# Performance work log

Measured on AMD Instinct MI355X. Metric: run time of the kernel, lower is better.

## Reference

```python
import jax, jax.numpy as jnp
import numpy as np

N0 = 260000  # all sampled nodes (hop-2 sources)
N1 = 60000   # hop-1 targets / hop-2 sources
N2 = 10000   # final batch targets
E1 = 1500000
E2 = 250000
DIN, DH, DOUT = 128, 256, 128


def sage_conv(x_src, x_tgt, src, dst, n_tgt, Wl, b, Wr):
    # mean aggregation of source features over incoming edges per target,
    # then lin_l(agg) + lin_r(x_tgt)  (PyG SAGEConv default, lin_r has no bias)
    msg = x_src[src]                                             # [E, d]
    agg = jax.ops.segment_sum(msg, dst, num_segments=n_tgt)      # [n_tgt, d]
    cnt = jax.ops.segment_sum(jnp.ones((src.shape[0], 1), x_src.dtype), dst,
                              num_segments=n_tgt)                # [n_tgt, 1]
    agg = agg / jnp.maximum(cnt, 1.0)
    return agg @ Wl + b + x_tgt @ Wr


def setup_inputs() -> dict:
    key = jax.random.key(0)
    ks = jax.random.split(key, 10)
    s = 1.0 / np.sqrt(DIN)
    s2 = 1.0 / np.sqrt(DH)
    return {
        "x": jax.random.normal(ks[0], (N0, DIN), dtype=jnp.float32),
        "W1l": jax.random.normal(ks[1], (DIN, DH), dtype=jnp.float32) * s,
        "b1": jnp.zeros((DH,), dtype=jnp.float32),
        "W1r": jax.random.normal(ks[2], (DIN, DH), dtype=jnp.float32) * s,
        "W2l": jax.random.normal(ks[3], (DH, DOUT), dtype=jnp.float32) * s2,
        "b2": jnp.zeros((DOUT,), dtype=jnp.float32),
        "W2r": jax.random.normal(ks[4], (DH, DOUT), dtype=jnp.float32) * s2,
        "src1": jax.random.randint(ks[5], (E1,), 0, N0, dtype=jnp.int32),
        "dst1": jax.random.randint(ks[6], (E1,), 0, N1, dtype=jnp.int32),
        "src2": jax.random.randint(ks[7], (E2,), 0, N1, dtype=jnp.int32),
        "dst2": jax.random.randint(ks[8], (E2,), 0, N2, dtype=jnp.int32),
    }


def reference(x, W1l, b1, W1r, W2l, b2, W2r, src1, dst1, src2, dst2):
    h = sage_conv(x, x[:N1], src1, dst1, N1, W1l, b1, W1r)  # [N1, DH]
    h = jax.nn.relu(h)
    out = sage_conv(h, h[:N2], src2, dst2, N2, W2l, b2, W2r)  # [N2, DOUT]
    return out
```

## Files before the change

### kernel.cpp

```cpp
#include <hip/hip_runtime.h>
#include <hip/hip_bf16.h>

#define N0 260000
#define N1 60000
#define N2 10000
#define E1 1500000
#define E2 250000
#define DIN 128
#define DH 256
#define DOUT 128
#define CAP 80

typedef __attribute__((ext_vector_type(8))) short bf16x8;
typedef __attribute__((ext_vector_type(4))) float f32x4;

#define MFMA16(a, b, c) __builtin_amdgcn_mfma_f32_16x16x32_bf16(a, b, c, 0, 0, 0)

__device__ inline float blo(unsigned u) { return __uint_as_float(u << 16); }
__device__ inline float bhi(unsigned u) { return __uint_as_float(u & 0xFFFF0000u); }
__device__ inline unsigned short f2b(float f) {
    unsigned u = __float_as_uint(f);
    return (unsigned short)((u + 0x7FFFu + ((u >> 16) & 1u)) >> 16);
}

#define BB_C1 256
#define BB_C2 64
#define BB_BLOCKS (8 * (BB_C1 + BB_C2))
#define P1ROWS (N1 / 8)
#define P2ROWS (N2 / 8)
#define CONVX_BLOCKS 16250
#define CONVW_BLOCKS 512
__global__ __launch_bounds__(256) void prep3(const float* __restrict__ x, unsigned short* __restrict__ xb,
                                             const float* __restrict__ W1l, const float* __restrict__ W1r,
                                             const float* __restrict__ W2l, const float* __restrict__ W2r,
                                             unsigned short* __restrict__ W1lt, unsigned short* __restrict__ W1rt,
                                             unsigned short* __restrict__ W2lt, unsigned short* __restrict__ W2rt,
                                             const int* __restrict__ src1, const int* __restrict__ dst1,
                                             int* __restrict__ cnt1, int* __restrict__ csr1,
                                             const int* __restrict__ src2, const int* __restrict__ dst2,
                                             int* __restrict__ cnt2, int* __restrict__ csr2,
                                             int use_xb) {
    int b = blockIdx.x;
    int t = threadIdx.x;
    if (b < BB_BLOCKS) {
        int part = b & 7, q = b >> 3;
        if (q < BB_C1) {
            int lo = part * P1ROWS, hi = lo + P1ROWS;
            const int4* d4 = reinterpret_cast<const int4*>(dst1);
            for (int i = q * 256 + t; i < E1 / 4; i += BB_C1 * 256) {
                int4 d = d4[i];
                int e0 = i * 4;
                if (d.x >= lo && d.x < hi) { int p = atomicAdd(&cnt1[d.x], 1); if (p < CAP) csr1[d.x * CAP + p] = src1[e0 + 0]; }
                if (d.y >= lo && d.y < hi) { int p = atomicAdd(&cnt1[d.y], 1); if (p < CAP) csr1[d.y * CAP + p] = src1[e0 + 1]; }
                if (d.z >= lo && d.z < hi) { int p = atomicAdd(&cnt1[d.z], 1); if (p < CAP) csr1[d.z * CAP + p] = src1[e0 + 2]; }
                if (d.w >= lo && d.w < hi) { int p = atomicAdd(&cnt1[d.w], 1); if (p < CAP) csr1[d.w * CAP + p] = src1[e0 + 3]; }
            }
        } else {
            q -= BB_C1;
            int lo = part * P2ROWS, hi = lo + P2ROWS;
            const int4* d4 = reinterpret_cast<const int4*>(dst2);
            for (int i = q * 256 + t; i < E2 / 4; i += BB_C2 * 256) {
                int4 d = d4[i];
                int e0 = i * 4;
                if (d.x >= lo && d.x < hi) { int p = atomicAdd(&cnt2[d.x], 1); if (p < CAP) csr2[d.x * CAP + p] = src2[e0 + 0]; }
                if (d.y >= lo && d.y < hi) { int p = atomicAdd(&cnt2[d.y], 1); if (p < CAP) csr2[d.y * CAP + p] = src2[e0 + 1]; }
                if (d.z >= lo && d.z < hi) { int p = atomicAdd(&cnt2[d.z], 1); if (p < CAP) csr2[d.z * CAP + p] = src2[e0 + 2]; }
                if (d.w >= lo && d.w < hi) { int p = atomicAdd(&cnt2[d.w], 1); if (p < CAP) csr2[d.w * CAP + p] = src2[e0 + 3]; }
            }
        }
    } else if (b < BB_BLOCKS + CONVX_BLOCKS) {
        if (!use_xb) return;
        size_t i = (size_t)(b - BB_BLOCKS) * 256 + t;
        const float4* xf = reinterpret_cast<const float4*>(x) + i * 2;
        float4 v0 = xf[0], v1 = xf[1];
        bf16x8 o;
        o[0] = (short)f2b(v0.x); o[1] = (short)f2b(v0.y); o[2] = (short)f2b(v0.z); o[3] = (short)f2b(v0.w);
        o[4] = (short)f2b(v1.x); o[5] = (short)f2b(v1.y); o[6] = (short)f2b(v1.z); o[7] = (short)f2b(v1.w);
        *reinterpret_cast<bf16x8*>(xb + i * 8) = o;
    } else {
        int tid = (b - BB_BLOCKS - CONVX_BLOCKS) * 256 + t;
        int seg = tid >> 15, idx = tid & 32767;
        if (seg == 0)      { int n = idx >> 7, k = idx & 127; W1lt[idx] = f2b(W1l[k * DH + n]); }
        else if (seg == 1) { int n = idx >> 7, k = idx & 127; W1rt[idx] = f2b(W1r[k * DH + n]); }
        else if (seg == 2) { int n = idx >> 8, k = idx & 255; W2lt[idx] = f2b(W2l[k * DOUT + n]); }
        else               { int n = idx >> 8, k = idx & 255; W2rt[idx] = f2b(W2r[k * DOUT + n]); }
    }
}

template <int XB>
__global__ __launch_bounds__(256) void agg_gemm1_k(const float* __restrict__ xf,
                                                   const unsigned short* __restrict__ xb,
                                                   const int* __restrict__ cnt,
                                                   const int* __restrict__ csr,
                                                   const unsigned short* __restrict__ Wlt,
                                                   const unsigned short* __restrict__ Wrt,
                                                   const float* __restrict__ b1,
                                                   unsigned short* __restrict__ hb) {
    __shared__ __align__(16) unsigned short lds[4352];
    const int XT0 = 2176;
    int t = threadIdx.x;
    int row0 = blockIdx.x * 16;
    int r = t >> 4, li = t & 15;
    int rawc = cnt[row0 + r];
    int deg = rawc > CAP ? CAP : rawc;
    int beg = (row0 + r) * CAP, end = beg + deg;
    float acc[8];
#pragma unroll
    for (int j = 0; j < 8; ++j) acc[j] = 0.0f;
    if (XB) {
        const uint4* base = reinterpret_cast<const uint4*>(xb);
        int e = beg;
        for (; e + 8 <= end; e += 8) {
            int4 sa = *reinterpret_cast<const int4*>(csr + e);
            int4 sb = *reinterpret_cast<const int4*>(csr + e + 4);
            uint4 v0 = base[(size_t)sa.x * 16 + li];
            uint4 v1 = base[(size_t)sa.y * 16 + li];
            uint4 v2 = base[(size_t)sa.z * 16 + li];
            uint4 v3 = base[(size_t)sa.w * 16 + li];
            uint4 v4 = base[(size_t)sb.x * 16 + li];
            uint4 v5 = base[(size_t)sb.y * 16 + li];
            uint4 v6 = base[(size_t)sb.z * 16 + li];
            uint4 v7 = base[(size_t)sb.w * 16 + li];
            acc[0] += blo(v0.x) + blo(v1.x) + blo(v2.x) + blo(v3.x) + blo(v4.x) + blo(v5.x) + blo(v6.x) + blo(v7.x);
            acc[1] += bhi(v0.x) + bhi(v1.x) + bhi(v2.x) + bhi(v3.x) + bhi(v4.x) + bhi(v5.x) + bhi(v6.x) + bhi(v7.x);
            acc[2] += blo(v0.y) + blo(v1.y) + blo(v2.y) + blo(v3.y) + blo(v4.y) + blo(v5.y) + blo(v6.y) + blo(v7.y);
            acc[3] += bhi(v0.y) + bhi(v1.y) + bhi(v2.y) + bhi(v3.y) + bhi(v4.y) + bhi(v5.y) + bhi(v6.y) + bhi(v7.y);
            acc[4] += blo(v0.z) + blo(v1.z) + blo(v2.z) + blo(v3.z) + blo(v4.z) + blo(v5.z) + blo(v6.z) + blo(v7.z);
            acc[5] += bhi(v0.z) + bhi(v1.z) + bhi(v2.z) + bhi(v3.z) + bhi(v4.z) + bhi(v5.z) + bhi(v6.z) + bhi(v7.z);
            acc[6] += blo(v0.w) + blo(v1.w) + blo(v2.w) + blo(v3.w) + blo(v4.w) + blo(v5.w) + blo(v6.w) + blo(v7.w);
            acc[7] += bhi(v0.w) + bhi(v1.w) + bhi(v2.w) + bhi(v3.w) + bhi(v4.w) + bhi(v5.w) + bhi(v6.w) + bhi(v7.w);
        }
        if (e + 4 <= end) {
            int4 sa = *reinterpret_cast<const int4*>(csr + e);
            uint4 v0 = base[(size_t)sa.x * 16 + li];
            uint4 v1 = base[(size_t)sa.y * 16 + li];
            uint4 v2 = base[(size_t)sa.z * 16 + li];
            uint4 v3 = base[(size_t)sa.w * 16 + li];
            acc[0] += blo(v0.x) + blo(v1.x) + blo(v2.x) + blo(v3.x);
            acc[1] += bhi(v0.x) + bhi(v1.x) + bhi(v2.x) + bhi(v3.x);
            acc[2] += blo(v0.y) + blo(v1.y) + blo(v2.y) + blo(v3.y);
            acc[3] += bhi(v0.y) + bhi(v1.y) + bhi(v2.y) + bhi(v3.y);
            acc[4] += blo(v0.z) + blo(v1.z) + blo(v2.z) + blo(v3.z);
            acc[5] += bhi(v0.z) + bhi(v1.z) + bhi(v2.z) + bhi(v3.z);
            acc[6] += blo(v0.w) + blo(v1.w) + blo(v2.w) + blo(v3.w);
            acc[7] += bhi(v0.w) + bhi(v1.w) + bhi(v2.w) + bhi(v3.w);
            e += 4;
        }
        for (; e < end; ++e) {
            int s = csr[e];
            uint4 v = base[(size_t)s * 16 + li];
            acc[0] += blo(v.x); acc[1] += bhi(v.x);
            acc[2] += blo(v.y); acc[3] += bhi(v.y);
            acc[4] += blo(v.z); acc[5] += bhi(v.z);
            acc[6] += blo(v.w); acc[7] += bhi(v.w);
        }
    } else {
        const float4* base = reinterpret_cast<const float4*>(xf);
        for (int e = beg; e < end; ++e) {
            int s = csr[e];
            float4 v0 = base[(size_t)s * 32 + li * 2];
            float4 v1 = base[(size_t)s * 32 + li * 2 + 1];
            acc[0] += v0.x; acc[1] += v0.y; acc[2] += v0.z; acc[3] += v0.w;
            acc[4] += v1.x; acc[5] += v1.y; acc[6] += v1.z; acc[7] += v1.w;
        }
    }
    float inv = 1.0f / fmaxf((float)rawc, 1.0f);
    bf16x8 av;
#pragma unroll
    for (int j = 0; j < 8; ++j) av[j] = (short)f2b(acc[j] * inv);
    *reinterpret_cast<bf16x8*>(&lds[r * 136 + li * 8]) = av;
    if (XB) {
        *reinterpret_cast<uint4*>(&lds[XT0 + r * 136 + li * 8]) =
            reinterpret_cast<const uint4*>(xb)[(size_t)(row0 + r) * 16 + li];
    } else {
        const float4* base = reinterpret_cast<const float4*>(xf);
        float4 v0 = base[(size_t)(row0 + r) * 32 + li * 2];
        float4 v1 = base[(size_t)(row0 + r) * 32 + li * 2 + 1];
        bf16x8 xv;
        xv[0] = (short)f2b(v0.x); xv[1] = (short)f2b(v0.y); xv[2] = (short)f2b(v0.z); xv[3] = (short)f2b(v0.w);
        xv[4] = (short)f2b(v1.x); xv[5] = (short)f2b(v1.y); xv[6] = (short)f2b(v1.z); xv[7] = (short)f2b(v1.w);
        *reinterpret_cast<bf16x8*>(&lds[XT0 + r * 136 + li * 8]) = xv;
    }
    __syncthreads();

    int l = t & 63, w = t >> 6;
    f32x4 c[4];
#pragma unroll
    for (int nt = 0; nt < 4; ++nt) c[nt] = (f32x4){0.f, 0.f, 0.f, 0.f};
    int arow = (l & 15) * 136;
    int colbase = w * 64 + (l & 15);
    int kbase = (l >> 4) * 8;
#pragma unroll
    for (int kk = 0; kk < 4; ++kk) {
        int goff = arow + (kk * 4 + (l >> 4)) * 8;
        bf16x8 af = *reinterpret_cast<const bf16x8*>(&lds[goff]);
        bf16x8 tf = *reinterpret_cast<const bf16x8*>(&lds[XT0 + goff]);
        int k = kk * 32 + kbase;
#pragma unroll
        for (int nt = 0; nt < 4; ++nt) {
            int n = colbase + nt * 16;
            bf16x8 wl = *reinterpret_cast<const bf16x8*>(&Wlt[n * DIN + k]);
            bf16x8 wr = *reinterpret_cast<const bf16x8*>(&Wrt[n * DIN + k]);
            c[nt] = MFMA16(af, wl, c[nt]);
            c[nt] = MFMA16(tf, wr, c[nt]);
        }
    }
    __syncthreads();
#pragma unroll
    for (int nt = 0; nt < 4; ++nt) {
        int col = colbase + nt * 16;
        float bias = b1[col];
#pragma unroll
        for (int j = 0; j < 4; ++j) {
            int rr = (l >> 4) * 4 + j;
            lds[rr * 264 + col] = f2b(fmaxf(c[nt][j] + bias, 0.0f));
        }
    }
    __syncthreads();
#pragma unroll
    for (int i = 0; i < 2; ++i) {
        int gi = t + i * 256;
        int rr = gi >> 5, g = gi & 31;
        *reinterpret_cast<uint4*>(&hb[(size_t)(row0 + rr) * 256 + g * 8]) =
            *reinterpret_cast<const uint4*>(&lds[rr * 264 + g * 8]);
    }
}

__global__ __launch_bounds__(512) void agg_gemm2_k(const unsigned short* __restrict__ hb,
                                                   const int* __restrict__ cnt,
                                                   const int* __restrict__ csr,
                                                   const unsigned short* __restrict__ Wlt,
                                                   const unsigned short* __restrict__ Wrt,
                                                   const float* __restrict__ b2,
                                                   float* __restrict__ out) {
    __shared__ __align__(16) unsigned short lds[8448];
    const int HT0 = 4224;
    int t = threadIdx.x;
    int row0 = blockIdx.x * 16;
    int r = t >> 5, li = t & 31;
    int rawc = cnt[row0 + r];
    int deg = rawc > CAP ? CAP : rawc;
    int beg = (row0 + r) * CAP, end = beg + deg;
    float acc[8];
#pragma unroll
    for (int j = 0; j < 8; ++j) acc[j] = 0.0f;
    const uint4* base = reinterpret_cast<const uint4*>(hb);
    int e = beg;
    for (; e + 8 <= end; e += 8) {
        int4 sa = *reinterpret_cast<const int4*>(csr + e);
        int4 sb = *reinterpret_cast<const int4*>(csr + e + 4);
        uint4 v0 = base[(size_t)sa.x * 32 + li];
        uint4 v1 = base[(size_t)sa.y * 32 + li];
        uint4 v2 = base[(size_t)sa.z * 32 + li];
        uint4 v3 = base[(size_t)sa.w * 32 + li];
        uint4 v4 = base[(size_t)sb.x * 32 + li];
        uint4 v5 = base[(size_t)sb.y * 32 + li];
        uint4 v6 = base[(size_t)sb.z * 32 + li];
        uint4 v7 = base[(size_t)sb.w * 32 + li];
        acc[0] += blo(v0.x) + blo(v1.x) + blo(v2.x) + blo(v3.x) + blo(v4.x) + blo(v5.x) + blo(v6.x) + blo(v7.x);
        acc[1] += bhi(v0.x) + bhi(v1.x) + bhi(v2.x) + bhi(v3.x) + bhi(v4.x) + bhi(v5.x) + bhi(v6.x) + bhi(v7.x);
        acc[2] += blo(v0.y) + blo(v1.y) + blo(v2.y) + blo(v3.y) + blo(v4.y) + blo(v5.y) + blo(v6.y) + blo(v7.y);
        acc[3] += bhi(v0.y) + bhi(v1.y) + bhi(v2.y) + bhi(v3.y) + bhi(v4.y) + bhi(v5.y) + bhi(v6.y) + bhi(v7.y);
        acc[4] += blo(v0.z) + blo(v1.z) + blo(v2.z) + blo(v3.z) + blo(v4.z) + blo(v5.z) + blo(v6.z) + blo(v7.z);
        acc[5] += bhi(v0.z) + bhi(v1.z) + bhi(v2.z) + bhi(v3.z) + bhi(v4.z) + bhi(v5.z) + bhi(v6.z) + bhi(v7.z);
        acc[6] += blo(v0.w) + blo(v1.w) + blo(v2.w) + blo(v3.w) + blo(v4.w) + blo(v5.w) + blo(v6.w) + blo(v7.w);
        acc[7] += bhi(v0.w) + bhi(v1.w) + bhi(v2.w) + bhi(v3.w) + bhi(v4.w) + bhi(v5.w) + bhi(v6.w) + bhi(v7.w);
    }
    if (e + 4 <= end) {
        int4 sa = *reinterpret_cast<const int4*>(csr + e);
        uint4 v0 = base[(size_t)sa.x * 32 + li];
        uint4 v1 = base[(size_t)sa.y * 32 + li];
        uint4 v2 = base[(size_t)sa.z * 32 + li];
        uint4 v3 = base[(size_t)sa.w * 32 + li];
        acc[0] += blo(v0.x) + blo(v1.x) + blo(v2.x) + blo(v3.x);
        acc[1] += bhi(v0.x) + bhi(v1.x) + bhi(v2.x) + bhi(v3.x);
        acc[2] += blo(v0.y) + blo(v1.y) + blo(v2.y) + blo(v3.y);
        acc[3] += bhi(v0.y) + bhi(v1.y) + bhi(v2.y) + bhi(v3.y);
        acc[4] += blo(v0.z) + blo(v1.z) + blo(v2.z) + blo(v3.z);
        acc[5] += bhi(v0.z) + bhi(v1.z) + bhi(v2.z) + bhi(v3.z);
        acc[6] += blo(v0.w) + blo(v1.w) + blo(v2.w) + blo(v3.w);
        acc[7] += bhi(v0.w) + bhi(v1.w) + bhi(v2.w) + bhi(v3.w);
        e += 4;
    }
    for (; e < end; ++e) {
        int s = csr[e];
        uint4 v = base[(size_t)s * 32 + li];
        acc[0] += blo(v.x); acc[1] += bhi(v.x);
        acc[2] += blo(v.y); acc[3] += bhi(v.y);
        acc[4] += blo(v.z); acc[5] += bhi(v.z);
        acc[6] += blo(v.w); acc[7] += bhi(v.w);
    }
    float inv = 1.0f / fmaxf((float)rawc, 1.0f);
    bf16x8 av;
#pragma unroll
    for (int j = 0; j < 8; ++j) av[j] = (short)f2b(acc[j] * inv);
    *reinterpret_cast<bf16x8*>(&lds[r * 264 + li * 8]) = av;
    *reinterpret_cast<uint4*>(&lds[HT0 + r * 264 + li * 8]) =
        reinterpret_cast<const uint4*>(&hb[(size_t)(row0 + r) * 256])[li];
    __syncthreads();

    int l = t & 63, w = t >> 6;
    f32x4 c = (f32x4){0.f, 0.f, 0.f, 0.f};
    int arow = (l & 15) * 264;
    int col = w * 16 + (l & 15);
    int kbase = (l >> 4) * 8;
#pragma unroll
    for (int kk = 0; kk < 8; ++kk) {
        int goff = arow + (kk * 4 + (l >> 4)) * 8;
        bf16x8 af = *reinterpret_cast<const bf16x8*>(&lds[goff]);
        bf16x8 hf = *reinterpret_cast<const bf16x8*>(&lds[HT0 + goff]);
        int k = kk * 32 + kbase;
        bf16x8 wl = *reinterpret_cast<const bf16x8*>(&Wlt[col * DH + k]);
        bf16x8 wr = *reinterpret_cast<const bf16x8*>(&Wrt[col * DH + k]);
        c = MFMA16(af, wl, c);
        c = MFMA16(hf, wr, c);
    }
    __syncthreads();
    float* O = reinterpret_cast<float*>(lds);
    float bias = b2[col];
#pragma unroll
    for (int j = 0; j < 4; ++j) {
        int rr = (l >> 4) * 4 + j;
        O[rr * 132 + col] = c[j] + bias;
    }
    __syncthreads();
    {
        int rr = t >> 5, c4 = t & 31;
        reinterpret_cast<float4*>(&out[(size_t)(row0 + rr) * 128])[c4] =
            reinterpret_cast<const float4*>(O)[rr * 33 + c4];
    }
}

extern "C" void kernel_launch(void* const* d_in, const int* in_sizes, int n_in,
                              void* d_out, int out_size, void* d_ws, size_t ws_size,
                              hipStream_t stream) {
    const float* x   = (const float*)d_in[0];
    const float* W1l = (const float*)d_in[1];
    const float* b1  = (const float*)d_in[2];
    const float* W1r = (const float*)d_in[3];
    const float* W2l = (const float*)d_in[4];
    const float* b2  = (const float*)d_in[5];
    const float* W2r = (const float*)d_in[6];
    const int* src1  = (const int*)d_in[7];
    const int* dst1  = (const int*)d_in[8];
    const int* src2  = (const int*)d_in[9];
    const int* dst2  = (const int*)d_in[10];
    float* out = (float*)d_out;

    char* ws = (char*)d_ws;
    size_t off = 0;
    auto alloc = [&](size_t bytes) { void* p = ws + off; off += (bytes + 255) & ~(size_t)255; return p; };
    int* cnt1    = (int*)alloc((size_t)N1 * 4);
    int* cnt2    = (int*)alloc((size_t)N2 * 4);
    int* csr1    = (int*)alloc((size_t)N1 * CAP * 4);
    int* csr2    = (int*)alloc((size_t)N2 * CAP * 4);
    unsigned short* W1lt = (unsigned short*)alloc((size_t)DIN * DH * 2);
    unsigned short* W1rt = (unsigned short*)alloc((size_t)DIN * DH * 2);
    unsigned short* W2lt = (unsigned short*)alloc((size_t)DH * DOUT * 2);
    unsigned short* W2rt = (unsigned short*)alloc((size_t)DH * DOUT * 2);
    unsigned short* hb   = (unsigned short*)alloc((size_t)N1 * DH * 2);
    unsigned short* xb   = (unsigned short*)alloc((size_t)N0 * DIN * 2);
    int use_xb = (off <= ws_size) ? 1 : 0;

    hipMemsetAsync(cnt1, 0, (size_t)((char*)cnt2 - (char*)cnt1) + (size_t)N2 * 4, stream);

    prep3<<<BB_BLOCKS + CONVX_BLOCKS + CONVW_BLOCKS, 256, 0, stream>>>(
        x, xb, W1l, W1r, W2l, W2r, W1lt, W1rt, W2lt, W2rt,
        src1, dst1, cnt1, csr1, src2, dst2, cnt2, csr2, use_xb);

    if (use_xb)
        agg_gemm1_k<1><<<N1 / 16, 256, 0, stream>>>(x, xb, cnt1, csr1, W1lt, W1rt, b1, hb);
    else
        agg_gemm1_k<0><<<N1 / 16, 256, 0, stream>>>(x, nullptr, cnt1, csr1, W1lt, W1rt, b1, hb);

    agg_gemm2_k<<<N2 / 16, 512, 0, stream>>>(hb, cnt2, csr2, W2lt, W2rt, b2, out);
}
```

Measured before the change: 248.7 us.

## Build CSR with per-block LDS counters instead of global atomics and memset

The CSR bucket build now uses 24 large blocks of 1024 threads. Each block owns a contiguous range of target rows, scans the whole edge list, and counts with shared-memory atomics before writing the counts to global memory. This removes the global atomic contention and the separate memset of the count arrays. In exchange, the build runs on only 24 blocks, and each block re-reads the full destination array serially, which can lengthen the critical path of the prep kernel.

```diff
diff --git a/kernel.cpp b/kernel.cpp
--- a/kernel.cpp
+++ b/kernel.cpp
@@ -23,54 +23,61 @@
     return (unsigned short)((u + 0x7FFFu + ((u >> 16) & 1u)) >> 16);
 }
 
-#define BB_C1 256
-#define BB_C2 64
-#define BB_BLOCKS (8 * (BB_C1 + BB_C2))
-#define P1ROWS (N1 / 8)
-#define P2ROWS (N2 / 8)
-#define CONVX_BLOCKS 16250
-#define CONVW_BLOCKS 512
-__global__ __launch_bounds__(256) void prep3(const float* __restrict__ x, unsigned short* __restrict__ xb,
-                                             const float* __restrict__ W1l, const float* __restrict__ W1r,
-                                             const float* __restrict__ W2l, const float* __restrict__ W2r,
-                                             unsigned short* __restrict__ W1lt, unsigned short* __restrict__ W1rt,
-                                             unsigned short* __restrict__ W2lt, unsigned short* __restrict__ W2rt,
-                                             const int* __restrict__ src1, const int* __restrict__ dst1,
-                                             int* __restrict__ cnt1, int* __restrict__ csr1,
-                                             const int* __restrict__ src2, const int* __restrict__ dst2,
-                                             int* __restrict__ cnt2, int* __restrict__ csr2,
-                                             int use_xb) {
+#define PT 1024
+#define NW1 16
+#define W1R (N1 / NW1)
+#define NW2 8
+#define W2R (N2 / NW2)
+#define BUILD_BLOCKS (NW1 + NW2)
+#define CONVX_BLOCKS ((N0 * DIN / 8 + PT - 1) / PT)
+#define CONVW_BLOCKS (131072 / PT)
+__global__ __launch_bounds__(1024) void prep4(const float* __restrict__ x, unsigned short* __restrict__ xb,
+                                              const float* __restrict__ W1l, const float* __restrict__ W1r,
+                                              const float* __restrict__ W2l, const float* __restrict__ W2r,
+                                              unsigned short* __restrict__ W1lt, unsigned short* __restrict__ W1rt,
+                                              unsigned short* __restrict__ W2lt, unsigned short* __restrict__ W2rt,
+                                              const int* __restrict__ src1, const int* __restrict__ dst1,
+                                              int* __restrict__ cnt1, int* __restrict__ csr1,
+                                              const int* __restrict__ src2, const int* __restrict__ dst2,
+                                              int* __restrict__ cnt2, int* __restrict__ csr2,
+                                              int use_xb) {
+    __shared__ int scnt[W1R];
     int b = blockIdx.x;
     int t = threadIdx.x;
-    if (b < BB_BLOCKS) {
-        int part = b & 7, q = b >> 3;
-        if (q < BB_C1) {
-            int lo = part * P1ROWS, hi = lo + P1ROWS;
-            const int4* d4 = reinterpret_cast<const int4*>(dst1);
-            for (int i = q * 256 + t; i < E1 / 4; i += BB_C1 * 256) {
-                int4 d = d4[i];
-                int e0 = i * 4;
-                if (d.x >= lo && d.x < hi) { int p = atomicAdd(&cnt1[d.x], 1); if (p < CAP) csr1[d.x * CAP + p] = src1[e0 + 0]; }
-                if (d.y >= lo && d.y < hi) { int p = atomicAdd(&cnt1[d.y], 1); if (p < CAP) csr1[d.y * CAP + p] = src1[e0 + 1]; }
-                if (d.z >= lo && d.z < hi) { int p = atomicAdd(&cnt1[d.z], 1); if (p < CAP) csr1[d.z * CAP + p] = src1[e0 + 2]; }
-                if (d.w >= lo && d.w < hi) { int p = atomicAdd(&cnt1[d.w], 1); if (p < CAP) csr1[d.w * CAP + p] = src1[e0 + 3]; }
-            }
-        } else {
-            q -= BB_C1;
-            int lo = part * P2ROWS, hi = lo + P2ROWS;
-            const int4* d4 = reinterpret_cast<const int4*>(dst2);
-            for (int i = q * 256 + t; i < E2 / 4; i += BB_C2 * 256) {
-                int4 d = d4[i];
-                int e0 = i * 4;
-                if (d.x >= lo && d.x < hi) { int p = atomicAdd(&cnt2[d.x], 1); if (p < CAP) csr2[d.x * CAP + p] = src2[e0 + 0]; }
-                if (d.y >= lo && d.y < hi) { int p = atomicAdd(&cnt2[d.y], 1); if (p < CAP) csr2[d.y * CAP + p] = src2[e0 + 1]; }
-                if (d.z >= lo && d.z < hi) { int p = atomicAdd(&cnt2[d.z], 1); if (p < CAP) csr2[d.z * CAP + p] = src2[e0 + 2]; }
-                if (d.w >= lo && d.w < hi) { int p = atomicAdd(&cnt2[d.w], 1); if (p < CAP) csr2[d.w * CAP + p] = src2[e0 + 3]; }
-            }
-        }
-    } else if (b < BB_BLOCKS + CONVX_BLOCKS) {
+    if (b < NW1) {
+        for (int j = t; j < W1R; j += PT) scnt[j] = 0;
+        __syncthreads();
+        int lo = b * W1R, hi = lo + W1R;
+        const int4* d4 = reinterpret_cast<const int4*>(dst1);
+        for (int i = t; i < E1 / 4; i += PT) {
+            int4 d = d4[i];
+            int e0 = i * 4;
+            if (d.x >= lo && d.x < hi) { int p = atomicAdd(&scnt[d.x - lo], 1); if (p < CAP) csr1[d.x * CAP + p] = src1[e0 + 0]; }
+            if (d.y >= lo && d.y < hi) { int p = atomicAdd(&scnt[d.y - lo], 1); if (p < CAP) csr1[d.y * CAP + p] = src1[e0 + 1]; }
+            if (d.z >= lo && d.z < hi) { int p = atomicAdd(&scnt[d.z - lo], 1); if (p < CAP) csr1[d.z * CAP + p] = src1[e0 + 2]; }
+            if (d.w >= lo && d.w < hi) { int p = atomicAdd(&scnt[d.w - lo], 1); if (p < CAP) csr1[d.w * CAP + p] = src1[e0 + 3]; }
+        }
+        __syncthreads();
+        for (int j = t; j < W1R; j += PT) cnt1[lo + j] = scnt[j];
+    } else if (b < BUILD_BLOCKS) {
+        for (int j = t; j < W2R; j += PT) scnt[j] = 0;
+        __syncthreads();
+        int lo = (b - NW1) * W2R, hi = lo + W2R;
+        const int4* d4 = reinterpret_cast<const int4*>(dst2);
+        for (int i = t; i < E2 / 4; i += PT) {
+            int4 d = d4[i];
+            int e0 = i * 4;
+            if (d.x >= lo && d.x < hi) { int p = atomicAdd(&scnt[d.x - lo], 1); if (p < CAP) csr2[d.x * CAP + p] = src2[e0 + 0]; }
+            if (d.y >= lo && d.y < hi) { int p = atomicAdd(&scnt[d.y - lo], 1); if (p < CAP) csr2[d.y * CAP + p] = src2[e0 + 1]; }
+            if (d.z >= lo && d.z < hi) { int p = atomicAdd(&scnt[d.z - lo], 1); if (p < CAP) csr2[d.z * CAP + p] = src2[e0 + 2]; }
+            if (d.w >= lo && d.w < hi) { int p = atomicAdd(&scnt[d.w - lo], 1); if (p < CAP) csr2[d.w * CAP + p] = src2[e0 + 3]; }
+        }
+        __syncthreads();
+        for (int j = t; j < W2R; j += PT) cnt2[lo + j] = scnt[j];
+    } else if (b < BUILD_BLOCKS + CONVX_BLOCKS) {
         if (!use_xb) return;
-        size_t i = (size_t)(b - BB_BLOCKS) * 256 + t;
+        size_t i = (size_t)(b - BUILD_BLOCKS) * PT + t;
+        if (i >= (size_t)N0 * DIN / 8) return;
         const float4* xf = reinterpret_cast<const float4*>(x) + i * 2;
         float4 v0 = xf[0], v1 = xf[1];
         bf16x8 o;
@@ -78,7 +85,7 @@
         o[4] = (short)f2b(v1.x); o[5] = (short)f2b(v1.y); o[6] = (short)f2b(v1.z); o[7] = (short)f2b(v1.w);
         *reinterpret_cast<bf16x8*>(xb + i * 8) = o;
     } else {
-        int tid = (b - BB_BLOCKS - CONVX_BLOCKS) * 256 + t;
+        int tid = (b - BUILD_BLOCKS - CONVX_BLOCKS) * PT + t;
         int seg = tid >> 15, idx = tid & 32767;
         if (seg == 0)      { int n = idx >> 7, k = idx & 127; W1lt[idx] = f2b(W1l[k * DH + n]); }
         else if (seg == 1) { int n = idx >> 7, k = idx & 127; W1rt[idx] = f2b(W1r[k * DH + n]); }
@@ -362,9 +369,8 @@
     unsigned short* xb   = (unsigned short*)alloc((size_t)N0 * DIN * 2);
     int use_xb = (off <= ws_size) ? 1 : 0;
 
-    hipMemsetAsync(cnt1, 0, (size_t)((char*)cnt2 - (char*)cnt1) + (size_t)N2 * 4, stream);
-
-    prep3<<<BB_BLOCKS + CONVX_BLOCKS + CONVW_BLOCKS, 256, 0, stream>>>(
+
+    prep4<<<BUILD_BLOCKS + CONVX_BLOCKS + CONVW_BLOCKS, 1024, 0, stream>>>(
         x, xb, W1l, W1r, W2l, W2r, W1lt, W1rt, W2lt, W2rt,
         src1, dst1, cnt1, csr1, src2, dst2, cnt2, csr2, use_xb);
 
```

New measurement: 756.9 us. 204% more time.
